# Optimization experiments

Hardware: AMD Instinct MI355X
Metric: run time of the kernel (lower is better)

Reference implementation:

```python
import jax, jax.numpy as jnp
import numpy as np

B, S, D, H, DC, HC = 2, 2048, 1024, 16, 64, 16  # batch, seq, hidden, heads, coord_dim, head_coord_dim
HD = D // H  # head_dim


def setup_inputs() -> dict:
    key = jax.random.key(0)
    ks = jax.random.split(key, 12)
    s = lambda fan_in: 1.0 / np.sqrt(fan_in)
    return {
        "hidden_states": jax.random.normal(ks[0], (B, S, D), jnp.float32),
        "coordinates": jax.random.normal(ks[1], (B, S, DC), jnp.float32),
        # weights stored [in, out] (used as x @ W + b, equivalent to torch Linear)
        "Wv": jax.random.uniform(ks[2], (D, D), jnp.float32, -s(D), s(D)),
        "bv": jax.random.uniform(ks[3], (D,), jnp.float32, -s(D), s(D)),
        "Wc": jax.random.uniform(ks[4], (DC, H * HC), jnp.float32, -s(DC), s(DC)),
        "bc": jax.random.uniform(ks[5], (H * HC,), jnp.float32, -s(DC), s(DC)),
        "Wn": jax.random.uniform(ks[6], (DC, DC), jnp.float32, -s(DC), s(DC)),
        "bn": jax.random.uniform(ks[7], (DC,), jnp.float32, -s(DC), s(DC)),
        "Wo": jax.random.uniform(ks[8], (D, D), jnp.float32, -s(D), s(D)),
        "bo": jax.random.uniform(ks[9], (D,), jnp.float32, -s(D), s(D)),
        "gamma": jax.random.normal(ks[10], (1, H, 1, 1), jnp.float32),
    }


def reference(hidden_states, coordinates, Wv, bv, Wc, bc, Wn, bn, Wo, bo, gamma):
    b, s, _ = hidden_states.shape
    # value: [B,H,S,HD]
    value = (hidden_states @ Wv + bv).reshape(b, s, H, HD).transpose(0, 2, 1, 3)
    # coord heads: [B,H,S,HC]
    z = (coordinates @ Wc + bc).reshape(b, s, H, HC).transpose(0, 2, 1, 3)
    z_sq = jnp.sum(z * z, axis=-1, keepdims=True)  # [B,H,S,1]
    sq_dist = z_sq + jnp.swapaxes(z_sq, -1, -2) - 2.0 * jnp.einsum("bhsc,bhtc->bhst", z, z)
    sq_dist = jnp.maximum(sq_dist, 0.0)
    g = jax.nn.softplus(gamma)  # [1,H,1,1]
    attn = jax.nn.softmax(-g * sq_dist, axis=-1)  # [B,H,S,S]
    out = jnp.einsum("bhst,bhtd->bhsd", attn, value)
    out = out.transpose(0, 2, 1, 3).reshape(b, s, D)
    updated_hidden = out @ Wo + bo
    updated_coords = coordinates @ Wn + bn
    return (updated_hidden, updated_coords)
```

## Files before the change

kernel.cpp:

```cpp
#include <hip/hip_runtime.h>
#include <hip/hip_bf16.h>

typedef short bf16x8 __attribute__((ext_vector_type(8)));
typedef float f32x4 __attribute__((ext_vector_type(4)));
typedef float f32x16 __attribute__((ext_vector_type(16)));
typedef unsigned short u16;
typedef unsigned int u32;

__device__ __forceinline__ u16 f2b(float f) {
  __hip_bfloat16 h = __float2bfloat16(f);
  return *reinterpret_cast<u16*>(&h);
}

#define MFMA16(a, b, c) __builtin_amdgcn_mfma_f32_16x16x32_bf16((a), (b), (c), 0, 0, 0)
#define MFMA32(a, b, c) __builtin_amdgcn_mfma_f32_32x32x16_bf16((a), (b), (c), 0, 0, 0)


__global__ void k_cvt(const float* __restrict__ in, u16* __restrict__ out, int n) {
  int i = (blockIdx.x * 256 + threadIdx.x) * 4;
  if (i >= n) return;
  float4 v = *reinterpret_cast<const float4*>(in + i);
  ushort4 o;
  o.x = f2b(v.x); o.y = f2b(v.y); o.z = f2b(v.z); o.w = f2b(v.w);
  *reinterpret_cast<ushort4*>(out + i) = o;
}

__global__ void k_wT(const float* __restrict__ W, u16* __restrict__ WT) {
  __shared__ float t[64][65];
  int tid = threadIdx.x;
  int r0 = (blockIdx.x & 15) << 6;
  int c0 = (blockIdx.x >> 4) << 6;
#pragma unroll
  for (int rep = 0; rep < 4; ++rep) {
    int e = tid + rep * 256;
    int r = e >> 4, c4 = (e & 15) << 2;
    float4 v = *reinterpret_cast<const float4*>(W + (size_t)(r0 + r) * 1024 + c0 + c4);
    t[r][c4] = v.x; t[r][c4 + 1] = v.y; t[r][c4 + 2] = v.z; t[r][c4 + 3] = v.w;
  }
  __syncthreads();
#pragma unroll
  for (int rep = 0; rep < 4; ++rep) {
    int e = tid + rep * 256;
    int c = e >> 4, r4 = (e & 15) << 2;
    ushort4 o;
    o.x = f2b(t[r4][c]); o.y = f2b(t[r4 + 1][c]);
    o.z = f2b(t[r4 + 2][c]); o.w = f2b(t[r4 + 3][c]);
    *reinterpret_cast<ushort4*>(WT + (size_t)(c0 + c) * 1024 + r0 + r4) = o;
  }
}

__global__ void k_z(const float* __restrict__ C, const float* __restrict__ Wc,
                    const float* __restrict__ bc, const float* __restrict__ gamma,
                    u16* __restrict__ Z, u16* __restrict__ Zg, u32* __restrict__ zghl) {
  int gid = blockIdx.x * 256 + threadIdx.x;
  int bs = gid >> 4, h = gid & 15;
  float gm = gamma[h];
  float g = (gm > 15.f) ? gm : log1pf(__expf(gm));
  float g2 = g * 1.4426950408889634f;
  float tg2 = 2.f * g2;
  const float* crow = C + (size_t)bs * 64;
  float acc[16];
#pragma unroll
  for (int c = 0; c < 16; ++c) acc[c] = bc[h * 16 + c];
  for (int k = 0; k < 64; ++k) {
    float cv = crow[k];
    const float* wr = Wc + (size_t)k * 256 + h * 16;
#pragma unroll
    for (int c = 0; c < 16; ++c) acc[c] = fmaf(cv, wr[c], acc[c]);
  }
  float sq = 0.f;
  u16 tz[16], tg[16];
#pragma unroll
  for (int c = 0; c < 16; ++c) {
    sq += acc[c] * acc[c];
    tz[c] = f2b(acc[c]);
    tg[c] = f2b(tg2 * acc[c]);
  }
  float x = -g2 * sq;
  u32 xu = __float_as_uint(x);
  float xh = __uint_as_float(xu & 0xFFFF0000u);
  u32 packed = (xu >> 16) | ((u32)f2b(x - xh) << 16);
  int b = bs >> 11, s = bs & 2047;
  int bh = (b << 4) + h;
  size_t ro = (((size_t)bh << 11) + s) * 16;
  *reinterpret_cast<uint4*>(Z + ro) = *reinterpret_cast<uint4*>(tz);
  *reinterpret_cast<uint4*>(Z + ro + 8) = *reinterpret_cast<uint4*>(tz + 8);
  *reinterpret_cast<uint4*>(Zg + ro) = *reinterpret_cast<uint4*>(tg);
  *reinterpret_cast<uint4*>(Zg + ro + 8) = *reinterpret_cast<uint4*>(tg + 8);
  zghl[((size_t)bh << 11) + s] = packed;
}

__global__ void k_coords(const float* __restrict__ C, const float* __restrict__ Wn,
                         const float* __restrict__ bn, float* __restrict__ out) {
  int gid = blockIdx.x * 256 + threadIdx.x;
  int bs = gid >> 6, c = gid & 63;
  const float* crow = C + (size_t)bs * 64;
  float acc = bn[c];
#pragma unroll 8
  for (int k = 0; k < 64; ++k) acc = fmaf(crow[k], Wn[k * 64 + c], acc);
  out[gid] = acc;
}

template <int OUTM>
__global__ __launch_bounds__(512, 4) void k_gemm(const u16* __restrict__ A,
                                                 const u16* __restrict__ BT,
                                                 const float* __restrict__ bias,
                                                 void* __restrict__ Cout,
                                                 int M, int N, int K) {
  __shared__ u16 As[128 * 64];
  __shared__ u16 Bs[64 * 64];
  int nbn = N >> 6;
  int bm = blockIdx.x / nbn, bn = blockIdx.x % nbn;
  int tid = threadIdx.x, lane = tid & 63, w = tid >> 6;
  int wm = w >> 1, wn = w & 1;
  int l15 = lane & 15, lg = lane >> 4;
  int lr = lane >> 3;
  int swc = (lane & 7) ^ lr;

  f32x4 acc[2][2];
#pragma unroll
  for (int mi = 0; mi < 2; ++mi)
#pragma unroll
    for (int ni = 0; ni < 2; ++ni) acc[mi][ni] = (f32x4){0.f, 0.f, 0.f, 0.f};

  const u16* Abase = A + (size_t)(bm * 128 + w * 8 + lr) * K + swc * 8;
  const u16* Bbase = BT + (size_t)(bn * 64 + w * 8 + lr) * K + swc * 8;
  int rsw = l15 & 7;

  for (int kk0 = 0; kk0 < K; kk0 += 64) {
    __syncthreads();
#pragma unroll
    for (int i = 0; i < 2; ++i)
      __builtin_amdgcn_global_load_lds(
          (const __attribute__((address_space(1))) u32*)(Abase + (size_t)(i * 64) * K + kk0),
          (__attribute__((address_space(3))) u32*)&As[(i * 64 + w * 8) * 64], 16, 0, 0);
    __builtin_amdgcn_global_load_lds(
        (const __attribute__((address_space(1))) u32*)(Bbase + kk0),
        (__attribute__((address_space(3))) u32*)&Bs[(w * 8) * 64], 16, 0, 0);
    __syncthreads();
#pragma unroll
    for (int kk = 0; kk < 2; ++kk) {
      int ch = (kk * 4 + lg) ^ rsw;
      bf16x8 af[2], bfr[2];
#pragma unroll
      for (int mi = 0; mi < 2; ++mi)
        af[mi] = *reinterpret_cast<const bf16x8*>(&As[(wm * 32 + mi * 16 + l15) * 64 + ch * 8]);
#pragma unroll
      for (int ni = 0; ni < 2; ++ni)
        bfr[ni] = *reinterpret_cast<const bf16x8*>(&Bs[(wn * 32 + ni * 16 + l15) * 64 + ch * 8]);
#pragma unroll
      for (int mi = 0; mi < 2; ++mi)
#pragma unroll
        for (int ni = 0; ni < 2; ++ni)
          acc[mi][ni] = MFMA16(af[mi], bfr[ni], acc[mi][ni]);
    }
  }
#pragma unroll
  for (int mi = 0; mi < 2; ++mi) {
#pragma unroll
    for (int ni = 0; ni < 2; ++ni) {
      int col = bn * 64 + wn * 32 + ni * 16 + l15;
      float bb = bias[col];
#pragma unroll
      for (int j = 0; j < 4; ++j) {
        int row = bm * 128 + wm * 32 + mi * 16 + lg * 4 + j;
        float v = acc[mi][ni][j] + bb;
        if (OUTM == 0) {
          reinterpret_cast<float*>(Cout)[(size_t)row * N + col] = v;
        } else {
          int b = row >> 11, s = row & 2047, h = col >> 6, hd = col & 63;
          reinterpret_cast<u16*>(Cout)[((((size_t)(b * 16 + h) << 11) | s) << 6) + hd] = f2b(v);
        }
      }
    }
  }
}

__global__ void k_vF(const u16* __restrict__ V, u16* __restrict__ VF) {
  __shared__ u16 t[64][72];
  int tid = threadIdx.x;
  int bh = blockIdx.x >> 5;
  int s0 = (blockIdx.x & 31) << 6;
#pragma unroll
  for (int rep = 0; rep < 2; ++rep) {
    int e = tid + rep * 256;
    int sl = e >> 3, seg = (e & 7) << 3;
    *reinterpret_cast<uint4*>(&t[sl][seg]) =
        *reinterpret_cast<const uint4*>(V + ((size_t)(bh * 2048 + s0 + sl) << 6) + seg);
  }
  __syncthreads();
  int tg0 = (blockIdx.x & 31) << 2;
#pragma unroll
  for (int rep = 0; rep < 2; ++rep) {
    int c = tid + rep * 256;
    int l = c & 63;
    int dh = (c >> 6) & 1;
    int tgl = c >> 7;
    int l31 = l & 31, hi = l >> 5;
    u16 tmp[8];
#pragma unroll
    for (int j = 0; j < 8; ++j) tmp[j] = t[tgl * 16 + hi * 8 + j][dh * 32 + l31];
    size_t off = ((((size_t)bh * 128 + tg0 + tgl) * 2 + dh) << 9) + (l << 3);
    *reinterpret_cast<uint4*>(VF + off) = *reinterpret_cast<uint4*>(tmp);
  }
}

__global__ __launch_bounds__(256, 4) void k_attn(const u16* __restrict__ Z,
                                                 const u16* __restrict__ Zg,
                                                 const u32* __restrict__ zghl,
                                                 const u16* __restrict__ VF,
                                                 u16* __restrict__ O) {
  __shared__ __align__(16) char smem[18944];
  float* psqf = reinterpret_cast<float*>(smem + 18432);

  int tid = threadIdx.x, lane = tid & 63, w = tid >> 6;
  int l31 = lane & 31, hi = lane >> 5;
  int hi4 = hi << 2, hi8 = hi << 3;
  int th = w >> 1, qh = w & 1, th32 = th << 5;
  int bh = blockIdx.x >> 5, qt = blockIdx.x & 31;
  int q0 = qt << 6;
  int h = bh & 15, bb = bh >> 4;

  const u16* Zb = Z + ((size_t)bh << 11) * 16;
  const u16* Zgb = Zg + ((size_t)bh << 11) * 16;
  const u32* ghl = zghl + ((size_t)bh << 11);
  const u16* VFb = VF + ((size_t)bh << 17);

  int q = (qh << 5) + l31;
  char* Prow = smem + q * 144;
  u32 psw = ((u32)(q >> 3) & 3u) << 4;

  bf16x8 zq2 = *reinterpret_cast<const bf16x8*>(Zgb + (size_t)(q0 + q) * 16 + hi8);

  u32 gq = ghl[q0 + q];
  uint4 abu = {0x3F803F80u, gq, 0u, 0u};
  if (hi) { abu.x = 0u; abu.y = 0u; }
  bf16x8 aug_b = *reinterpret_cast<bf16x8*>(&abu);

  uint4 aqu = {0u, 0x3F803F80u, 0u, 0u};
  if (hi) aqu.y = 0u;
  bf16x8 aug_q = *reinterpret_cast<bf16x8*>(&aqu);
  f32x16 qpart = MFMA32(aug_q, aug_b, (f32x16){});

  const u16* zap = Zb + (size_t)(th32 + l31) * 16 + hi8;
  const u32* xtp = ghl + th32 + l31;
  const u16* vwp = VFb + ((size_t)(th * 2) << 10) + (lane << 3);

  f32x16 oacc0 = {}, oacc1 = {};
  f32x4 psacc = {};

  bf16x8 zA_c = *reinterpret_cast<const bf16x8*>(zap);
  u32 zhl_c = xtp[0];
  bf16x8 vb00_c = *reinterpret_cast<const bf16x8*>(vwp);
  bf16x8 vb10_c = *reinterpret_cast<const bf16x8*>(vwp + 512);

#pragma unroll 2
  for (int tt = 0; tt < 32; ++tt) {
    const int t0 = tt << 6;
    char* Pr = Prow + ((tt & 1) ? 9216 : 0);
    const u16* vtb = vwp + (tt << 12);
    bf16x8 vb01 = *reinterpret_cast<const bf16x8*>(vtb + 1024);
    bf16x8 vb11 = *reinterpret_cast<const bf16x8*>(vtb + 1024 + 512);
    bf16x8 zA_n = zA_c, vb00_n = vb00_c, vb10_n = vb10_c;
    u32 zhl_n = zhl_c;
    if (tt < 31) {
      zA_n = *reinterpret_cast<const bf16x8*>(zap + (size_t)(t0 + 64) * 16);
      zhl_n = xtp[t0 + 64];
      vb00_n = *reinterpret_cast<const bf16x8*>(vtb + 4096);
      vb10_n = *reinterpret_cast<const bf16x8*>(vtb + 4096 + 512);
    }

    uint4 aau = {hi ? 0u : zhl_c, 0u, 0u, 0u};
    bf16x8 aug_a = *reinterpret_cast<bf16x8*>(&aau);

    f32x16 sc = MFMA32(aug_a, aug_b, qpart);
    sc = MFMA32(zA_c, zq2, sc);

#pragma unroll
    for (int g4 = 0; g4 < 4; ++g4) {
      float e0 = fminf(sc[g4 * 4 + 0], 0.f);
      float e1 = fminf(sc[g4 * 4 + 1], 0.f);
      float e2 = fminf(sc[g4 * 4 + 2], 0.f);
      float e3 = fminf(sc[g4 * 4 + 3], 0.f);
      float p0 = __builtin_amdgcn_exp2f(e0);
      float p1 = __builtin_amdgcn_exp2f(e1);
      float p2 = __builtin_amdgcn_exp2f(e2);
      float p3 = __builtin_amdgcn_exp2f(e3);
      psacc[0] += p0; psacc[1] += p1; psacc[2] += p2; psacc[3] += p3;
      u32 pk0, pk1;
      asm("v_cvt_pk_bf16_f32 %0, %1, %2" : "=v"(pk0) : "v"(p0), "v"(p1));
      asm("v_cvt_pk_bf16_f32 %0, %1, %2" : "=v"(pk1) : "v"(p2), "v"(p3));
      uint2 pkv = {pk0, pk1};
      int tcol = th32 + (g4 << 3) + hi4;
      *reinterpret_cast<uint2*>(Pr + (((u32)(tcol << 1)) ^ psw)) = pkv;
    }

    bf16x8 pa0 = *reinterpret_cast<const bf16x8*>(Pr + (((u32)((th32 + hi8) << 1)) ^ psw));
    bf16x8 pa1 = *reinterpret_cast<const bf16x8*>(Pr + (((u32)((th32 + 16 + hi8) << 1)) ^ psw));

    oacc0 = MFMA32(pa0, vb00_c, oacc0);
    oacc1 = MFMA32(pa0, vb10_c, oacc1);
    oacc0 = MFMA32(pa1, vb01, oacc0);
    oacc1 = MFMA32(pa1, vb11, oacc1);

    zA_c = zA_n; zhl_c = zhl_n; vb00_c = vb00_n; vb10_c = vb10_n;
  }

  float psum = (psacc[0] + psacc[1]) + (psacc[2] + psacc[3]);

  psum += __shfl_xor(psum, 32, 64);
  __syncthreads();
  if (w >= 2) {
    char* dst = smem + (w - 2) * 8192 + lane * 16;
#pragma unroll
    for (int c = 0; c < 4; ++c) {
      f32x4 v = {oacc0[c * 4 + 0], oacc0[c * 4 + 1], oacc0[c * 4 + 2], oacc0[c * 4 + 3]};
      *reinterpret_cast<f32x4*>(dst + c * 1024) = v;
    }
#pragma unroll
    for (int c = 0; c < 4; ++c) {
      f32x4 v = {oacc1[c * 4 + 0], oacc1[c * 4 + 1], oacc1[c * 4 + 2], oacc1[c * 4 + 3]};
      *reinterpret_cast<f32x4*>(dst + (c + 4) * 1024) = v;
    }
  }
  if (lane < 32) psqf[w * 32 + l31] = psum;
  __syncthreads();
  if (w < 2) {
    const char* src = smem + w * 8192 + lane * 16;
#pragma unroll
    for (int c = 0; c < 4; ++c) {
      f32x4 v = *reinterpret_cast<const f32x4*>(src + c * 1024);
      oacc0[c * 4 + 0] += v[0]; oacc0[c * 4 + 1] += v[1];
      oacc0[c * 4 + 2] += v[2]; oacc0[c * 4 + 3] += v[3];
    }
#pragma unroll
    for (int c = 0; c < 4; ++c) {
      f32x4 v = *reinterpret_cast<const f32x4*>(src + (c + 4) * 1024);
      oacc1[c * 4 + 0] += v[0]; oacc1[c * 4 + 1] += v[1];
      oacc1[c * 4 + 2] += v[2]; oacc1[c * 4 + 3] += v[3];
    }
#pragma unroll
    for (int g4 = 0; g4 < 4; ++g4) {
      f32x4 a = *reinterpret_cast<const f32x4*>(&psqf[qh * 32 + (g4 << 3) + hi4]);
      f32x4 b2 = *reinterpret_cast<const f32x4*>(&psqf[(qh + 2) * 32 + (g4 << 3) + hi4]);
#pragma unroll
      for (int j = 0; j < 4; ++j) {
        float inv = __builtin_amdgcn_rcpf(a[j] + b2[j]);
        int qrow = (g4 << 3) + hi4 + j;
        int srow = q0 + (qh << 5) + qrow;
        u16* orow = O + ((size_t)(bb * 2048 + srow) << 10) + h * 64 + l31;
        orow[0] = f2b(oacc0[g4 * 4 + j] * inv);
        orow[32] = f2b(oacc1[g4 * 4 + j] * inv);
      }
    }
  }
}

extern "C" void kernel_launch(void* const* d_in, const int* in_sizes, int n_in,
                              void* d_out, int out_size, void* d_ws, size_t ws_size,
                              hipStream_t stream) {
  const float* hs     = (const float*)d_in[0];
  const float* coords = (const float*)d_in[1];
  const float* Wv     = (const float*)d_in[2];
  const float* bv     = (const float*)d_in[3];
  const float* Wc     = (const float*)d_in[4];
  const float* bc     = (const float*)d_in[5];
  const float* Wn     = (const float*)d_in[6];
  const float* bn     = (const float*)d_in[7];
  const float* Wo     = (const float*)d_in[8];
  const float* bo     = (const float*)d_in[9];
  const float* gamma  = (const float*)d_in[10];
  float* out_h = (float*)d_out;
  float* out_c = out_h + 4194304;

  char* ws = (char*)d_ws;
  u16*   HSb  = (u16*)(ws + 0);
  u16*   O    = (u16*)(ws + 0);
  u16*   WvT  = (u16*)(ws + 8388608);
  u16*   WoT  = (u16*)(ws + 10485760);
  u16*   Zw   = (u16*)(ws + 12582912);
  u16*   Zgw  = (u16*)(ws + 14680064);
  u32*   zghl = (u32*)(ws + 16777216);
  u16*   Vw   = (u16*)(ws + 17039360);
  u16*   VFw  = (u16*)(ws + 25427968);

  k_cvt<<<4096, 256, 0, stream>>>(hs, HSb, 4194304);
  k_wT<<<256, 256, 0, stream>>>(Wv, WvT);
  k_wT<<<256, 256, 0, stream>>>(Wo, WoT);
  k_z<<<256, 256, 0, stream>>>(coords, Wc, bc, gamma, Zw, Zgw, zghl);
  k_gemm<1><<<512, 512, 0, stream>>>(HSb, WvT, bv, Vw, 4096, 1024, 1024);
  k_vF<<<1024, 256, 0, stream>>>(Vw, VFw);
  k_attn<<<1024, 256, 0, stream>>>(Zw, Zgw, zghl, VFw, O);
  k_gemm<0><<<512, 512, 0, stream>>>(O, WoT, bo, out_h, 4096, 1024, 1024);
  k_coords<<<1024, 256, 0, stream>>>(coords, Wn, bn, out_c);
}
```

Baseline: 122.9 us.

## Fuse V fragment layout into GEMM epilogue and double query tile per attention block

The V-projection GEMM epilogue now writes bf16 values directly in the MFMA fragment layout the attention kernel consumes, which removes the separate k_vF transpose kernel and its intermediate buffer round trip. The attention kernel now processes 128 queries per block: each wave handles two 32-query sub-tiles and reuses the loaded key/value fragments across both, and the grid is halved. In exchange it uses more registers and shared memory (launch bounds lowered to 2 blocks per SIMD) and uses a new XOR swizzle for the P tile. Occupancy and parallelism drop with 512 blocks.

```diff
diff --git a/kernel.cpp b/kernel.cpp
--- a/kernel.cpp
+++ b/kernel.cpp
@@ -160,65 +160,43 @@
 #pragma unroll
     for (int ni = 0; ni < 2; ++ni) {
       int col = bn * 64 + wn * 32 + ni * 16 + l15;
-      float bb = bias[col];
-#pragma unroll
-      for (int j = 0; j < 4; ++j) {
-        int row = bm * 128 + wm * 32 + mi * 16 + lg * 4 + j;
-        float v = acc[mi][ni][j] + bb;
-        if (OUTM == 0) {
-          reinterpret_cast<float*>(Cout)[(size_t)row * N + col] = v;
-        } else {
-          int b = row >> 11, s = row & 2047, h = col >> 6, hd = col & 63;
-          reinterpret_cast<u16*>(Cout)[((((size_t)(b * 16 + h) << 11) | s) << 6) + hd] = f2b(v);
+      float bv = bias[col];
+      if (OUTM == 0) {
+#pragma unroll
+        for (int j = 0; j < 4; ++j) {
+          int row = bm * 128 + wm * 32 + mi * 16 + lg * 4 + j;
+          reinterpret_cast<float*>(Cout)[(size_t)row * N + col] = acc[mi][ni][j] + bv;
         }
+      } else {
+        int row0 = bm * 128 + wm * 32 + mi * 16 + lg * 4;
+        int b = row0 >> 11, tg = (row0 >> 4) & 127;
+        int hi_ = lg >> 1, jb = (lg & 1) << 2;
+        int h = col >> 6, hd = col & 63, dh = hd >> 5, lv = hd & 31;
+        size_t addr = ((((size_t)(b * 16 + h) * 128 + tg) * 2 + dh) << 9) +
+                      ((hi_ * 32 + lv) << 3) + jb;
+        ushort4 o;
+        o.x = f2b(acc[mi][ni][0] + bv); o.y = f2b(acc[mi][ni][1] + bv);
+        o.z = f2b(acc[mi][ni][2] + bv); o.w = f2b(acc[mi][ni][3] + bv);
+        *reinterpret_cast<ushort4*>(reinterpret_cast<u16*>(Cout) + addr) = o;
       }
     }
   }
 }
 
-__global__ void k_vF(const u16* __restrict__ V, u16* __restrict__ VF) {
-  __shared__ u16 t[64][72];
-  int tid = threadIdx.x;
-  int bh = blockIdx.x >> 5;
-  int s0 = (blockIdx.x & 31) << 6;
-#pragma unroll
-  for (int rep = 0; rep < 2; ++rep) {
-    int e = tid + rep * 256;
-    int sl = e >> 3, seg = (e & 7) << 3;
-    *reinterpret_cast<uint4*>(&t[sl][seg]) =
-        *reinterpret_cast<const uint4*>(V + ((size_t)(bh * 2048 + s0 + sl) << 6) + seg);
-  }
-  __syncthreads();
-  int tg0 = (blockIdx.x & 31) << 2;
-#pragma unroll
-  for (int rep = 0; rep < 2; ++rep) {
-    int c = tid + rep * 256;
-    int l = c & 63;
-    int dh = (c >> 6) & 1;
-    int tgl = c >> 7;
-    int l31 = l & 31, hi = l >> 5;
-    u16 tmp[8];
-#pragma unroll
-    for (int j = 0; j < 8; ++j) tmp[j] = t[tgl * 16 + hi * 8 + j][dh * 32 + l31];
-    size_t off = ((((size_t)bh * 128 + tg0 + tgl) * 2 + dh) << 9) + (l << 3);
-    *reinterpret_cast<uint4*>(VF + off) = *reinterpret_cast<uint4*>(tmp);
-  }
-}
-
-__global__ __launch_bounds__(256, 4) void k_attn(const u16* __restrict__ Z,
+__global__ __launch_bounds__(256, 2) void k_attn(const u16* __restrict__ Z,
                                                  const u16* __restrict__ Zg,
                                                  const u32* __restrict__ zghl,
                                                  const u16* __restrict__ VF,
                                                  u16* __restrict__ O) {
-  __shared__ __align__(16) char smem[18944];
-  float* psqf = reinterpret_cast<float*>(smem + 18432);
+  __shared__ __align__(16) char smem[33792];
+  float* psqf = reinterpret_cast<float*>(smem + 32768);
 
   int tid = threadIdx.x, lane = tid & 63, w = tid >> 6;
   int l31 = lane & 31, hi = lane >> 5;
   int hi4 = hi << 2, hi8 = hi << 3;
-  int th = w >> 1, qh = w & 1, th32 = th << 5;
-  int bh = blockIdx.x >> 5, qt = blockIdx.x & 31;
-  int q0 = qt << 6;
+  int th = w & 1, qh = w >> 1, th32 = th << 5;
+  int bh = blockIdx.x >> 4, qt = blockIdx.x & 15;
+  int q0 = qt << 7;
   int h = bh & 15, bb = bh >> 4;
 
   const u16* Zb = Z + ((size_t)bh << 11) * 16;
@@ -226,131 +204,168 @@
   const u32* ghl = zghl + ((size_t)bh << 11);
   const u16* VFb = VF + ((size_t)bh << 17);
 
-  int q = (qh << 5) + l31;
-  char* Prow = smem + q * 144;
-  u32 psw = ((u32)(q >> 3) & 3u) << 4;
-
-  bf16x8 zq2 = *reinterpret_cast<const bf16x8*>(Zgb + (size_t)(q0 + q) * 16 + hi8);
-
-  u32 gq = ghl[q0 + q];
-  uint4 abu = {0x3F803F80u, gq, 0u, 0u};
-  if (hi) { abu.x = 0u; abu.y = 0u; }
-  bf16x8 aug_b = *reinterpret_cast<bf16x8*>(&abu);
+  int qx0 = (qh << 6) + l31;
+  int qx1 = qx0 + 32;
+
+  bf16x8 zq2_0 = *reinterpret_cast<const bf16x8*>(Zgb + (size_t)(q0 + qx0) * 16 + hi8);
+  bf16x8 zq2_1 = *reinterpret_cast<const bf16x8*>(Zgb + (size_t)(q0 + qx1) * 16 + hi8);
+
+  u32 gq0 = ghl[q0 + qx0], gq1 = ghl[q0 + qx1];
+  uint4 ab0 = {0x3F803F80u, gq0, 0u, 0u};
+  uint4 ab1 = {0x3F803F80u, gq1, 0u, 0u};
+  if (hi) { ab0.x = 0u; ab0.y = 0u; ab1.x = 0u; ab1.y = 0u; }
+  bf16x8 aug_b0 = *reinterpret_cast<bf16x8*>(&ab0);
+  bf16x8 aug_b1 = *reinterpret_cast<bf16x8*>(&ab1);
 
   uint4 aqu = {0u, 0x3F803F80u, 0u, 0u};
   if (hi) aqu.y = 0u;
   bf16x8 aug_q = *reinterpret_cast<bf16x8*>(&aqu);
-  f32x16 qpart = MFMA32(aug_q, aug_b, (f32x16){});
+  f32x16 qpart0 = MFMA32(aug_q, aug_b0, (f32x16){});
+  f32x16 qpart1 = MFMA32(aug_q, aug_b1, (f32x16){});
 
   const u16* zap = Zb + (size_t)(th32 + l31) * 16 + hi8;
   const u32* xtp = ghl + th32 + l31;
-  const u16* vwp = VFb + ((size_t)(th * 2) << 10) + (lane << 3);
-
-  f32x16 oacc0 = {}, oacc1 = {};
-  f32x4 psacc = {};
+  const u16* vwp = VFb + ((size_t)th << 11) + ((size_t)lane << 3);
+
+  f32x16 oacc00 = {}, oacc01 = {}, oacc10 = {}, oacc11 = {};
+  f32x4 ps0 = {}, ps1 = {};
+
+  int swz = (l31 ^ (l31 >> 2)) & 3;
+  char* pbase = smem + (w << 12) + l31 * 64;
 
   bf16x8 zA_c = *reinterpret_cast<const bf16x8*>(zap);
   u32 zhl_c = xtp[0];
-  bf16x8 vb00_c = *reinterpret_cast<const bf16x8*>(vwp);
-  bf16x8 vb10_c = *reinterpret_cast<const bf16x8*>(vwp + 512);
 
 #pragma unroll 2
   for (int tt = 0; tt < 32; ++tt) {
     const int t0 = tt << 6;
-    char* Pr = Prow + ((tt & 1) ? 9216 : 0);
     const u16* vtb = vwp + (tt << 12);
-    bf16x8 vb01 = *reinterpret_cast<const bf16x8*>(vtb + 1024);
-    bf16x8 vb11 = *reinterpret_cast<const bf16x8*>(vtb + 1024 + 512);
-    bf16x8 zA_n = zA_c, vb00_n = vb00_c, vb10_n = vb10_c;
+    bf16x8 vb00 = *reinterpret_cast<const bf16x8*>(vtb);
+    bf16x8 vb01 = *reinterpret_cast<const bf16x8*>(vtb + 512);
+    bf16x8 vb10 = *reinterpret_cast<const bf16x8*>(vtb + 1024);
+    bf16x8 vb11 = *reinterpret_cast<const bf16x8*>(vtb + 1536);
+    bf16x8 zA_n = zA_c;
     u32 zhl_n = zhl_c;
     if (tt < 31) {
       zA_n = *reinterpret_cast<const bf16x8*>(zap + (size_t)(t0 + 64) * 16);
       zhl_n = xtp[t0 + 64];
-      vb00_n = *reinterpret_cast<const bf16x8*>(vtb + 4096);
-      vb10_n = *reinterpret_cast<const bf16x8*>(vtb + 4096 + 512);
     }
 
     uint4 aau = {hi ? 0u : zhl_c, 0u, 0u, 0u};
     bf16x8 aug_a = *reinterpret_cast<bf16x8*>(&aau);
 
-    f32x16 sc = MFMA32(aug_a, aug_b, qpart);
-    sc = MFMA32(zA_c, zq2, sc);
-
-#pragma unroll
-    for (int g4 = 0; g4 < 4; ++g4) {
-      float e0 = fminf(sc[g4 * 4 + 0], 0.f);
-      float e1 = fminf(sc[g4 * 4 + 1], 0.f);
-      float e2 = fminf(sc[g4 * 4 + 2], 0.f);
-      float e3 = fminf(sc[g4 * 4 + 3], 0.f);
-      float p0 = __builtin_amdgcn_exp2f(e0);
-      float p1 = __builtin_amdgcn_exp2f(e1);
-      float p2 = __builtin_amdgcn_exp2f(e2);
-      float p3 = __builtin_amdgcn_exp2f(e3);
-      psacc[0] += p0; psacc[1] += p1; psacc[2] += p2; psacc[3] += p3;
-      u32 pk0, pk1;
-      asm("v_cvt_pk_bf16_f32 %0, %1, %2" : "=v"(pk0) : "v"(p0), "v"(p1));
-      asm("v_cvt_pk_bf16_f32 %0, %1, %2" : "=v"(pk1) : "v"(p2), "v"(p3));
-      uint2 pkv = {pk0, pk1};
-      int tcol = th32 + (g4 << 3) + hi4;
-      *reinterpret_cast<uint2*>(Pr + (((u32)(tcol << 1)) ^ psw)) = pkv;
-    }
-
-    bf16x8 pa0 = *reinterpret_cast<const bf16x8*>(Pr + (((u32)((th32 + hi8) << 1)) ^ psw));
-    bf16x8 pa1 = *reinterpret_cast<const bf16x8*>(Pr + (((u32)((th32 + 16 + hi8) << 1)) ^ psw));
-
-    oacc0 = MFMA32(pa0, vb00_c, oacc0);
-    oacc1 = MFMA32(pa0, vb10_c, oacc1);
-    oacc0 = MFMA32(pa1, vb01, oacc0);
-    oacc1 = MFMA32(pa1, vb11, oacc1);
-
-    zA_c = zA_n; zhl_c = zhl_n; vb00_c = vb00_n; vb10_c = vb10_n;
-  }
-
-  float psum = (psacc[0] + psacc[1]) + (psacc[2] + psacc[3]);
-
-  psum += __shfl_xor(psum, 32, 64);
+    f32x16 sc0 = MFMA32(aug_a, aug_b0, qpart0);
+    sc0 = MFMA32(zA_c, zq2_0, sc0);
+    f32x16 sc1 = MFMA32(aug_a, aug_b1, qpart1);
+    sc1 = MFMA32(zA_c, zq2_1, sc1);
+
+    char* pb = pbase + ((tt & 1) << 14);
+#pragma unroll
+    for (int g = 0; g < 4; ++g) {
+      int cb = ((g ^ swz) << 4) + (hi << 3);
+      {
+        float e0 = fminf(sc0[g * 4 + 0], 0.f), e1 = fminf(sc0[g * 4 + 1], 0.f);
+        float e2 = fminf(sc0[g * 4 + 2], 0.f), e3 = fminf(sc0[g * 4 + 3], 0.f);
+        float p0 = __builtin_amdgcn_exp2f(e0), p1 = __builtin_amdgcn_exp2f(e1);
+        float p2 = __builtin_amdgcn_exp2f(e2), p3 = __builtin_amdgcn_exp2f(e3);
+        ps0[0] += p0; ps0[1] += p1; ps0[2] += p2; ps0[3] += p3;
+        u32 pk0, pk1;
+        asm("v_cvt_pk_bf16_f32 %0, %1, %2" : "=v"(pk0) : "v"(p0), "v"(p1));
+        asm("v_cvt_pk_bf16_f32 %0, %1, %2" : "=v"(pk1) : "v"(p2), "v"(p3));
+        uint2 pkv = {pk0, pk1};
+        *reinterpret_cast<uint2*>(pb + cb) = pkv;
+      }
+      {
+        float e0 = fminf(sc1[g * 4 + 0], 0.f), e1 = fminf(sc1[g * 4 + 1], 0.f);
+        float e2 = fminf(sc1[g * 4 + 2], 0.f), e3 = fminf(sc1[g * 4 + 3], 0.f);
+        float p0 = __builtin_amdgcn_exp2f(e0), p1 = __builtin_amdgcn_exp2f(e1);
+        float p2 = __builtin_amdgcn_exp2f(e2), p3 = __builtin_amdgcn_exp2f(e3);
+        ps1[0] += p0; ps1[1] += p1; ps1[2] += p2; ps1[3] += p3;
+        u32 pk0, pk1;
+        asm("v_cvt_pk_bf16_f32 %0, %1, %2" : "=v"(pk0) : "v"(p0), "v"(p1));
+        asm("v_cvt_pk_bf16_f32 %0, %1, %2" : "=v"(pk1) : "v"(p2), "v"(p3));
+        uint2 pkv = {pk0, pk1};
+        *reinterpret_cast<uint2*>(pb + 2048 + cb) = pkv;
+      }
+    }
+
+    int c0b = (((0 * 2 + hi) ^ swz) << 4);
+    int c1b = (((1 * 2 + hi) ^ swz) << 4);
+    bf16x8 pa00 = *reinterpret_cast<const bf16x8*>(pb + c0b);
+    bf16x8 pa01 = *reinterpret_cast<const bf16x8*>(pb + c1b);
+    bf16x8 pa10 = *reinterpret_cast<const bf16x8*>(pb + 2048 + c0b);
+    bf16x8 pa11 = *reinterpret_cast<const bf16x8*>(pb + 2048 + c1b);
+
+    oacc00 = MFMA32(pa00, vb00, oacc00);
+    oacc01 = MFMA32(pa00, vb01, oacc01);
+    oacc10 = MFMA32(pa10, vb00, oacc10);
+    oacc11 = MFMA32(pa10, vb01, oacc11);
+    oacc00 = MFMA32(pa01, vb10, oacc00);
+    oacc01 = MFMA32(pa01, vb11, oacc01);
+    oacc10 = MFMA32(pa11, vb10, oacc10);
+    oacc11 = MFMA32(pa11, vb11, oacc11);
+
+    zA_c = zA_n; zhl_c = zhl_n;
+  }
+
+  float psum0 = (ps0[0] + ps0[1]) + (ps0[2] + ps0[3]);
+  float psum1 = (ps1[0] + ps1[1]) + (ps1[2] + ps1[3]);
+  psum0 += __shfl_xor(psum0, 32, 64);
+  psum1 += __shfl_xor(psum1, 32, 64);
+
   __syncthreads();
-  if (w >= 2) {
-    char* dst = smem + (w - 2) * 8192 + lane * 16;
-#pragma unroll
-    for (int c = 0; c < 4; ++c) {
-      f32x4 v = {oacc0[c * 4 + 0], oacc0[c * 4 + 1], oacc0[c * 4 + 2], oacc0[c * 4 + 3]};
-      *reinterpret_cast<f32x4*>(dst + c * 1024) = v;
-    }
-#pragma unroll
-    for (int c = 0; c < 4; ++c) {
-      f32x4 v = {oacc1[c * 4 + 0], oacc1[c * 4 + 1], oacc1[c * 4 + 2], oacc1[c * 4 + 3]};
-      *reinterpret_cast<f32x4*>(dst + (c + 4) * 1024) = v;
-    }
-  }
-  if (lane < 32) psqf[w * 32 + l31] = psum;
+  if (th == 1) {
+    char* dst = smem + ((w >> 1) << 14) + lane * 16;
+#pragma unroll
+    for (int r = 0; r < 4; ++r) {
+      *reinterpret_cast<f32x4*>(dst + (0 + r) * 1024) =
+          (f32x4){oacc00[r * 4], oacc00[r * 4 + 1], oacc00[r * 4 + 2], oacc00[r * 4 + 3]};
+      *reinterpret_cast<f32x4*>(dst + (4 + r) * 1024) =
+          (f32x4){oacc01[r * 4], oacc01[r * 4 + 1], oacc01[r * 4 + 2], oacc01[r * 4 + 3]};
+      *reinterpret_cast<f32x4*>(dst + (8 + r) * 1024) =
+          (f32x4){oacc10[r * 4], oacc10[r * 4 + 1], oacc10[r * 4 + 2], oacc10[r * 4 + 3]};
+      *reinterpret_cast<f32x4*>(dst + (12 + r) * 1024) =
+          (f32x4){oacc11[r * 4], oacc11[r * 4 + 1], oacc11[r * 4 + 2], oacc11[r * 4 + 3]};
+    }
+  }
+  if (lane < 32) {
+    psqf[(w * 2 + 0) * 32 + l31] = psum0;
+    psqf[(w * 2 + 1) * 32 + l31] = psum1;
+  }
   __syncthreads();
-  if (w < 2) {
-    const char* src = smem + w * 8192 + lane * 16;
-#pragma unroll
-    for (int c = 0; c < 4; ++c) {
-      f32x4 v = *reinterpret_cast<const f32x4*>(src + c * 1024);
-      oacc0[c * 4 + 0] += v[0]; oacc0[c * 4 + 1] += v[1];
-      oacc0[c * 4 + 2] += v[2]; oacc0[c * 4 + 3] += v[3];
-    }
-#pragma unroll
-    for (int c = 0; c < 4; ++c) {
-      f32x4 v = *reinterpret_cast<const f32x4*>(src + (c + 4) * 1024);
-      oacc1[c * 4 + 0] += v[0]; oacc1[c * 4 + 1] += v[1];
-      oacc1[c * 4 + 2] += v[2]; oacc1[c * 4 + 3] += v[3];
-    }
-#pragma unroll
-    for (int g4 = 0; g4 < 4; ++g4) {
-      f32x4 a = *reinterpret_cast<const f32x4*>(&psqf[qh * 32 + (g4 << 3) + hi4]);
-      f32x4 b2 = *reinterpret_cast<const f32x4*>(&psqf[(qh + 2) * 32 + (g4 << 3) + hi4]);
+  if (th == 0) {
+    const char* src = smem + ((w >> 1) << 14) + lane * 16;
+#pragma unroll
+    for (int r = 0; r < 4; ++r) {
+      f32x4 v0 = *reinterpret_cast<const f32x4*>(src + (0 + r) * 1024);
+      f32x4 v1 = *reinterpret_cast<const f32x4*>(src + (4 + r) * 1024);
+      f32x4 v2 = *reinterpret_cast<const f32x4*>(src + (8 + r) * 1024);
+      f32x4 v3 = *reinterpret_cast<const f32x4*>(src + (12 + r) * 1024);
 #pragma unroll
       for (int j = 0; j < 4; ++j) {
-        float inv = __builtin_amdgcn_rcpf(a[j] + b2[j]);
-        int qrow = (g4 << 3) + hi4 + j;
-        int srow = q0 + (qh << 5) + qrow;
-        u16* orow = O + ((size_t)(bb * 2048 + srow) << 10) + h * 64 + l31;
-        orow[0] = f2b(oacc0[g4 * 4 + j] * inv);
-        orow[32] = f2b(oacc1[g4 * 4 + j] * inv);
+        oacc00[r * 4 + j] += v0[j];
+        oacc01[r * 4 + j] += v1[j];
+        oacc10[r * 4 + j] += v2[j];
+        oacc11[r * 4 + j] += v3[j];
+      }
+    }
+#pragma unroll
+    for (int qbk = 0; qbk < 2; ++qbk) {
+#pragma unroll
+      for (int g = 0; g < 4; ++g) {
+        f32x4 a = *reinterpret_cast<const f32x4*>(&psqf[(w * 2 + qbk) * 32 + (g << 3) + hi4]);
+        f32x4 b2 = *reinterpret_cast<const f32x4*>(&psqf[((w + 1) * 2 + qbk) * 32 + (g << 3) + hi4]);
+#pragma unroll
+        for (int j = 0; j < 4; ++j) {
+          float inv = __builtin_amdgcn_rcpf(a[j] + b2[j]);
+          int qrow = (g << 3) + hi4 + j;
+          int srow = q0 + (qh << 6) + (qbk << 5) + qrow;
+          u16* orow = O + ((size_t)(bb * 2048 + srow) << 10) + h * 64 + l31;
+          float v0 = (qbk ? oacc10[g * 4 + j] : oacc00[g * 4 + j]);
+          float v1 = (qbk ? oacc11[g * 4 + j] : oacc01[g * 4 + j]);
+          orow[0] = f2b(v0 * inv);
+          orow[32] = f2b(v1 * inv);
+        }
       }
     }
   }
@@ -381,16 +396,14 @@
   u16*   Zw   = (u16*)(ws + 12582912);
   u16*   Zgw  = (u16*)(ws + 14680064);
   u32*   zghl = (u32*)(ws + 16777216);
-  u16*   Vw   = (u16*)(ws + 17039360);
-  u16*   VFw  = (u16*)(ws + 25427968);
+  u16*   VFw  = (u16*)(ws + 17039360);
 
   k_cvt<<<4096, 256, 0, stream>>>(hs, HSb, 4194304);
   k_wT<<<256, 256, 0, stream>>>(Wv, WvT);
   k_wT<<<256, 256, 0, stream>>>(Wo, WoT);
   k_z<<<256, 256, 0, stream>>>(coords, Wc, bc, gamma, Zw, Zgw, zghl);
-  k_gemm<1><<<512, 512, 0, stream>>>(HSb, WvT, bv, Vw, 4096, 1024, 1024);
-  k_vF<<<1024, 256, 0, stream>>>(Vw, VFw);
-  k_attn<<<1024, 256, 0, stream>>>(Zw, Zgw, zghl, VFw, O);
+  k_gemm<1><<<512, 512, 0, stream>>>(HSb, WvT, bv, VFw, 4096, 1024, 1024);
+  k_attn<<<512, 256, 0, stream>>>(Zw, Zgw, zghl, VFw, O);
   k_gemm<0><<<512, 512, 0, stream>>>(O, WoT, bo, out_h, 4096, 1024, 1024);
   k_coords<<<1024, 256, 0, stream>>>(coords, Wn, bn, out_c);
 }
```

Result: faster. 114.7 us (-6.7%).
